# Kernel tuning notes

Measured on AMD Instinct MI355X. Metric: run time of the kernel, lower is better.

The kernel has to match this reference:

```python
import jax, jax.numpy as jnp
import numpy as np

N_NODES = 100000
N_EDGES = 1600000
D = 128          # in_dim == out_dim
H = 8            # num_heads
DH = D // H      # head dim = 16
DFF = 2 * D
EPS_LN = 1e-5


def _ln(x, g, b):
    mu = jnp.mean(x, axis=-1, keepdims=True)
    var = jnp.var(x, axis=-1, keepdims=True)
    return (x - mu) * jax.lax.rsqrt(var + EPS_LN) * g + b


def setup_inputs() -> dict:
    key = jax.random.key(0)
    ks = jax.random.split(key, 12)
    s = 1.0 / np.sqrt(D)
    inp = {
        "h": jax.random.normal(ks[0], (N_NODES, D), jnp.float32),
        "src": jax.random.randint(ks[1], (N_EDGES,), 0, N_NODES, jnp.int32),
        "dst": jax.random.randint(ks[2], (N_EDGES,), 0, N_NODES, jnp.int32),
        "Wq": jax.random.normal(ks[3], (D, D), jnp.float32) * s,
        "Wk": jax.random.normal(ks[4], (D, D), jnp.float32) * s,
        "Wv": jax.random.normal(ks[5], (D, D), jnp.float32) * s,
        "Wo": jax.random.normal(ks[6], (D, D), jnp.float32) * s,
        "bo": jnp.zeros((D,), jnp.float32),
        "ln1_g": jnp.ones((D,), jnp.float32),
        "ln1_b": jnp.zeros((D,), jnp.float32),
        "W1": jax.random.normal(ks[7], (D, DFF), jnp.float32) * s,
        "b1": jnp.zeros((DFF,), jnp.float32),
        "W2": jax.random.normal(ks[8], (DFF, D), jnp.float32) * (1.0 / np.sqrt(DFF)),
        "b2": jnp.zeros((D,), jnp.float32),
        "ln2_g": jnp.ones((D,), jnp.float32),
        "ln2_b": jnp.zeros((D,), jnp.float32),
    }
    return inp


def reference(h, src, dst, Wq, Wk, Wv, Wo, bo, ln1_g, ln1_b, W1, b1, W2, b2, ln2_g, ln2_b):
    n = h.shape[0]
    # Q/K/V projections (no bias), split into heads: [N, H, DH]
    Q = (h @ Wq).reshape(n, H, DH)
    K = (h @ Wk).reshape(n, H, DH)
    V = (h @ Wv).reshape(n, H, DH)

    # edge-wise attention score: K[src] . Q[dst] / sqrt(DH), exp-clamped
    score = jnp.einsum("ehd,ehd->eh", K[src], Q[dst]) / np.sqrt(DH)  # [E, H]
    score = jnp.exp(jnp.clip(score, -5.0, 5.0))

    # weighted message sum + normalizer via segment reduce over dst
    m = V[src] * score[:, :, None]                                   # [E, H, DH]
    wV = jax.ops.segment_sum(m, dst, num_segments=n)                 # [N, H, DH]
    z = jax.ops.segment_sum(score, dst, num_segments=n)              # [N, H]

    h_attn = (wV / (z[:, :, None] + 1e-6)).reshape(n, D)

    # output projection + residual + LN
    x = h + (h_attn @ Wo + bo)
    x = _ln(x, ln1_g, ln1_b)

    # FFN + residual + LN
    y = jax.nn.relu(x @ W1 + b1) @ W2 + b2
    x = _ln(x + y, ln2_g, ln2_b)
    return x
```

## Files before the change

### kernel.cpp

```cpp
#include <hip/hip_runtime.h>
#include <hip/hip_bf16.h>
#include <math.h>


typedef __attribute__((ext_vector_type(8))) short bf16x8;
typedef __attribute__((ext_vector_type(4))) float f32x4;

#define BSHIFT 9
#define BSIZE  512

template<int K, bool AF32, bool RELU, bool LN, bool RESID, bool BIAS, bool YW>
__global__ __launch_bounds__(256)
void gemm_mfma(const void* __restrict__ Ap, int lda,
               const __hip_bfloat16* __restrict__ Bt, int ldbt,
               const float* __restrict__ bias, const float* __restrict__ resid,
               const float* __restrict__ lng, const float* __restrict__ lnb,
               float* __restrict__ Cf, __hip_bfloat16* __restrict__ Cb, int ldc,
               size_t bt_ystride, size_t cb_ystride, int N)
{
    constexpr int CK = 128;
    __shared__ unsigned short As[64 * 136];
    __shared__ unsigned short Bs[128 * 136];

    const int tid  = threadIdx.x;
    const int row0 = blockIdx.x * 64;
    int col0 = 0;
    if (YW) { Bt += blockIdx.y * bt_ystride; Cb += blockIdx.y * cb_ystride; }
    else    col0 = blockIdx.y * 128;

    const int wave = tid >> 6, lane = tid & 63;
    const int quad = lane >> 4, l15 = lane & 15;

    f32x4 acc[8];
    #pragma unroll
    for (int t = 0; t < 8; ++t) acc[t] = (f32x4)0.f;

    for (int kc = 0; kc < K; kc += CK) {
        #pragma unroll
        for (int it = 0; it < 4; ++it) {
            int i = tid + it * 256;
            int r = i >> 4, kb = i & 15;
            int rg = row0 + r; if (rg > N - 1) rg = N - 1;
            if (AF32) {
                const float* Af = (const float*)Ap;
                const float4 f0 = *(const float4*)&Af[(size_t)rg * lda + kc + kb * 8];
                const float4 f1 = *(const float4*)&Af[(size_t)rg * lda + kc + kb * 8 + 4];
                __hip_bfloat162 b01 = __float22bfloat162_rn(make_float2(f0.x, f0.y));
                __hip_bfloat162 b23 = __float22bfloat162_rn(make_float2(f0.z, f0.w));
                __hip_bfloat162 b45 = __float22bfloat162_rn(make_float2(f1.x, f1.y));
                __hip_bfloat162 b67 = __float22bfloat162_rn(make_float2(f1.z, f1.w));
                uint4 u;
                u.x = *(unsigned*)&b01; u.y = *(unsigned*)&b23;
                u.z = *(unsigned*)&b45; u.w = *(unsigned*)&b67;
                *(uint4*)&As[r * 136 + kb * 8] = u;
            } else {
                const __hip_bfloat16* Ab = (const __hip_bfloat16*)Ap;
                *(uint4*)&As[r * 136 + kb * 8] =
                    *(const uint4*)&Ab[(size_t)rg * lda + kc + kb * 8];
            }
        }
        #pragma unroll
        for (int it = 0; it < 8; ++it) {
            int i = tid + it * 256;
            int r = i >> 4, kb = i & 15;
            *(uint4*)&Bs[r * 136 + kb * 8] =
                *(const uint4*)&Bt[(size_t)(col0 + r) * ldbt + kc + kb * 8];
        }
        __syncthreads();
        const unsigned short* ap = &As[(wave * 16 + l15) * 136 + quad * 8];
        const unsigned short* bp = &Bs[l15 * 136 + quad * 8];
        #pragma unroll
        for (int ks = 0; ks < 4; ++ks) {
            bf16x8 a = *(const bf16x8*)(ap + ks * 32);
            #pragma unroll
            for (int t = 0; t < 8; ++t) {
                bf16x8 b = *(const bf16x8*)(bp + t * 16 * 136 + ks * 32);
                acc[t] = __builtin_amdgcn_mfma_f32_16x16x32_bf16(a, b, acc[t], 0, 0, 0);
            }
        }
        __syncthreads();
    }

    const int rbase = row0 + wave * 16 + quad * 4;

    float vals[8][4];
    #pragma unroll
    for (int t = 0; t < 8; ++t) {
        float bv = BIAS ? bias[col0 + t * 16 + l15] : 0.f;
        #pragma unroll
        for (int i = 0; i < 4; ++i) vals[t][i] = acc[t][i] + bv;
    }
    if (RESID) {
        #pragma unroll
        for (int i = 0; i < 4; ++i) {
            int row = rbase + i;
            if (row < N) {
                #pragma unroll
                for (int t = 0; t < 8; ++t)
                    vals[t][i] += resid[(size_t)row * 128 + t * 16 + l15];
            }
        }
    }
    if (RELU) {
        #pragma unroll
        for (int t = 0; t < 8; ++t)
            #pragma unroll
            for (int i = 0; i < 4; ++i) vals[t][i] = fmaxf(vals[t][i], 0.f);
    }
    if (LN) {
        #pragma unroll
        for (int i = 0; i < 4; ++i) {
            float s = 0.f, sq = 0.f;
            #pragma unroll
            for (int t = 0; t < 8; ++t) { float v = vals[t][i]; s += v; sq += v * v; }
            s  += __shfl_xor(s, 1);  s  += __shfl_xor(s, 2);
            s  += __shfl_xor(s, 4);  s  += __shfl_xor(s, 8);
            sq += __shfl_xor(sq, 1); sq += __shfl_xor(sq, 2);
            sq += __shfl_xor(sq, 4); sq += __shfl_xor(sq, 8);
            float m  = s * (1.f / 128.f);
            float rs = rsqrtf(sq * (1.f / 128.f) - m * m + 1e-5f);
            #pragma unroll
            for (int t = 0; t < 8; ++t) {
                float g = lng[t * 16 + l15], b = lnb[t * 16 + l15];
                vals[t][i] = (vals[t][i] - m) * rs * g + b;
            }
        }
    }
    #pragma unroll
    for (int i = 0; i < 4; ++i) {
        int row = rbase + i;
        if (row >= N) continue;
        if (Cf) {
            #pragma unroll
            for (int t = 0; t < 8; ++t)
                Cf[(size_t)row * ldc + col0 + t * 16 + l15] = vals[t][i];
        }
        if (Cb) {
            #pragma unroll
            for (int t = 0; t < 8; ++t)
                Cb[(size_t)row * ldc + col0 + t * 16 + l15] = __float2bfloat16(vals[t][i]);
        }
    }
}

struct WArgs {
    const float* src[6];
    __hip_bfloat16* dst[6];
    int R[6], C[6];
};
__global__ __launch_bounds__(256)
void cast_w(WArgs wa)
{
    int w = blockIdx.y;
    int R = wa.R[w], C = wa.C[w];
    int i = blockIdx.x * 256 + threadIdx.x;
    if (i >= R * C) return;
    int sh = (C == 256) ? 8 : 7;
    int r = i >> sh, c = i & (C - 1);
    wa.dst[w][(size_t)c * R + r] = __float2bfloat16(wa.src[w][i]);
}


__global__ __launch_bounds__(256)
void bucket_hist(const int* __restrict__ dst, int* __restrict__ bCnt,
                 int E, int chunk, int NB)
{
    __shared__ int bh[256];
    const int t = threadIdx.x;
    bh[t] = 0;
    __syncthreads();
    const int s0 = blockIdx.x * chunk;
    const int s1 = min(E, s0 + chunk);
    for (int i = s0 + t; i < s1; i += 256)
        atomicAdd(&bh[dst[i] >> BSHIFT], 1);
    __syncthreads();
    if (t < NB && bh[t]) atomicAdd(&bCnt[t], bh[t]);
}

__global__ __launch_bounds__(256)
void bucket_scan(const int* __restrict__ bCnt, int* __restrict__ bBase,
                 int* __restrict__ gCur, int* __restrict__ rowStart,
                 int N, int E, int NB)
{
    __shared__ int wsum[4];
    const int t = threadIdx.x, lane = t & 63, wv = t >> 6;
    int v = (t < NB) ? bCnt[t] : 0;
    const int s = v;
    for (int off = 1; off < 64; off <<= 1) {
        int u = __shfl_up(v, off);
        if (lane >= off) v += u;
    }
    if (lane == 63) wsum[wv] = v;
    __syncthreads();
    int add = 0;
    for (int w = 0; w < wv; ++w) add += wsum[w];
    const int excl = v + add - s;
    if (t <= NB) bBase[t] = excl;
    if (t < NB)  gCur[t]  = excl;
    if (t == 0)  rowStart[N] = E;
}

__global__ __launch_bounds__(256)
void partition_kernel(const int* __restrict__ src, const int* __restrict__ dst,
                      int* __restrict__ gCur, uint2* __restrict__ P,
                      int E, int chunk, int NB)
{
    __shared__ int ch[256];
    __shared__ int cur[256];
    const int t = threadIdx.x;
    ch[t] = 0;
    __syncthreads();
    const int s0 = blockIdx.x * chunk;
    const int s1 = min(E, s0 + chunk);
    for (int i = s0 + t; i < s1; i += 256)
        atomicAdd(&ch[dst[i] >> BSHIFT], 1);
    __syncthreads();
    if (t < NB) {
        int c = ch[t];
        cur[t] = c ? atomicAdd(&gCur[t], c) : 0;
    }
    __syncthreads();
    for (int i = s0 + t; i < s1; i += 256) {
        int d = dst[i];
        int pos = atomicAdd(&cur[d >> BSHIFT], 1);
        P[pos] = make_uint2((unsigned)src[i], (unsigned)d);
    }
}

__global__ __launch_bounds__(256)
void bucket_scatter(const uint2* __restrict__ P, const int* __restrict__ bBase,
                    int* __restrict__ rowStart, int* __restrict__ esrc, int N)
{
    __shared__ int hist[BSIZE];
    __shared__ int cur[BSIZE];
    __shared__ int wsum[4];

    const int b  = blockIdx.x;
    const int t  = threadIdx.x;
    const int d0 = b << BSHIFT;
    const int bb  = bBase[b];
    const int cnt = bBase[b + 1] - bb;

    hist[t] = 0; hist[t + 256] = 0;
    __syncthreads();
    for (int i = t; i < cnt; i += 256)
        atomicAdd(&hist[(int)P[bb + i].y - d0], 1);
    __syncthreads();

    {
        const int a0 = hist[2 * t], a1 = hist[2 * t + 1];
        int v = a0 + a1;
        const int s = v;
        const int lane = t & 63, wv = t >> 6;
        for (int off = 1; off < 64; off <<= 1) {
            int u = __shfl_up(v, off);
            if (lane >= off) v += u;
        }
        if (lane == 63) wsum[wv] = v;
        __syncthreads();
        int add = 0;
        for (int w = 0; w < wv; ++w) add += wsum[w];
        const int exclT = v + add - s;
        cur[2 * t]     = exclT;
        cur[2 * t + 1] = exclT + a0;
    }
    __syncthreads();
    for (int i = t; i < BSIZE; i += 256) {
        int d = d0 + i;
        if (d < N) rowStart[d] = bb + cur[i];
    }
    __syncthreads();
    for (int i = t; i < cnt; i += 256) {
        uint2 p = P[bb + i];
        int pos = atomicAdd(&cur[(int)p.y - d0], 1);
        esrc[bb + pos] = (int)p.x;
    }
}

__global__ __launch_bounds__(256)
void aggregate_kernel(__hip_bfloat16* __restrict__ Q,
                      const __hip_bfloat16* __restrict__ Km,
                      const __hip_bfloat16* __restrict__ V,
                      const int* __restrict__ esrc,
                      const int* __restrict__ rowStart, int N)
{
    const int lane = threadIdx.x & 63;
    const int wid  = threadIdx.x >> 6;
    const int d    = blockIdx.x * 4 + wid;
    if (d >= N) return;

    const int l5   = lane & 31;
    const int half = lane >> 5;

    const uint2* K2 = (const uint2*)Km;
    const uint2* V2 = (const uint2*)V;
    uint2*       Q2 = (uint2*)Q;

    const uint2 qraw = Q2[(unsigned)d * 32u + (unsigned)l5];
    const float q0 = __uint_as_float(qraw.x << 16);
    const float q1 = __uint_as_float(qraw.x & 0xffff0000u);
    const float q2 = __uint_as_float(qraw.y << 16);
    const float q3 = __uint_as_float(qraw.y & 0xffff0000u);

    const int beg = rowStart[d];
    const int end = rowStart[d + 1];

    float a0 = 0.f, a1 = 0.f, a2 = 0.f, a3 = 0.f, zacc = 0.f;
    const float S = 0.36067376022224085f;
    const float C = 7.2134752044448170f;

    for (int base = beg; base < end; base += 64) {
        int n = end - base; if (n > 64) n = 64;
        int mysrc = (lane < n) ? esrc[base + lane] : 0;
        const int nf = n >> 1;
        int bidx = half;
        for (int j = 0; j < nf; ++j, bidx += 2) {
            const int s = __shfl(mysrc, bidx);
            const unsigned off = (unsigned)s * 32u + (unsigned)l5;
            const uint2 kraw = K2[off];
            const uint2 vraw = V2[off];
            float p = __uint_as_float(kraw.x << 16)         * q0
                    + __uint_as_float(kraw.x & 0xffff0000u) * q1
                    + __uint_as_float(kraw.y << 16)         * q2
                    + __uint_as_float(kraw.y & 0xffff0000u) * q3;
            p += __shfl_xor(p, 1);
            p += __shfl_xor(p, 2);
            const float tt = fminf(C, fmaxf(-C, p * S));
            const float se = exp2f(tt);
            a0 += __uint_as_float(vraw.x << 16)         * se;
            a1 += __uint_as_float(vraw.x & 0xffff0000u) * se;
            a2 += __uint_as_float(vraw.y << 16)         * se;
            a3 += __uint_as_float(vraw.y & 0xffff0000u) * se;
            zacc += se;
        }
        if (n & 1) {
            const int s = __shfl(mysrc, n - 1);
            const unsigned off = (unsigned)s * 32u + (unsigned)l5;
            const uint2 kraw = K2[off];
            const uint2 vraw = V2[off];
            float p = __uint_as_float(kraw.x << 16)         * q0
                    + __uint_as_float(kraw.x & 0xffff0000u) * q1
                    + __uint_as_float(kraw.y << 16)         * q2
                    + __uint_as_float(kraw.y & 0xffff0000u) * q3;
            p += __shfl_xor(p, 1);
            p += __shfl_xor(p, 2);
            const float tt = fminf(C, fmaxf(-C, p * S));
            float se = exp2f(tt);
            se = half ? 0.f : se;
            a0 += __uint_as_float(vraw.x << 16)         * se;
            a1 += __uint_as_float(vraw.x & 0xffff0000u) * se;
            a2 += __uint_as_float(vraw.y << 16)         * se;
            a3 += __uint_as_float(vraw.y & 0xffff0000u) * se;
            zacc += se;
        }
    }

    a0 += __shfl_xor(a0, 32); a1 += __shfl_xor(a1, 32);
    a2 += __shfl_xor(a2, 32); a3 += __shfl_xor(a3, 32);
    zacc += __shfl_xor(zacc, 32);

    if (half == 0) {
        const float inv = 1.0f / (zacc + 1e-6f);
        __hip_bfloat162 p0 = __float22bfloat162_rn(make_float2(a0 * inv, a1 * inv));
        __hip_bfloat162 p1 = __float22bfloat162_rn(make_float2(a2 * inv, a3 * inv));
        uint2 o;
        o.x = *(unsigned*)&p0;
        o.y = *(unsigned*)&p1;
        Q2[(unsigned)d * 32u + (unsigned)l5] = o;
    }
}

extern "C" void kernel_launch(void* const* d_in, const int* in_sizes, int n_in,
                              void* d_out, int out_size, void* d_ws, size_t ws_size,
                              hipStream_t stream)
{
    const float* h    = (const float*)d_in[0];
    const int*   src  = (const int*)  d_in[1];
    const int*   dst  = (const int*)  d_in[2];
    const float* Wq   = (const float*)d_in[3];
    const float* Wk   = (const float*)d_in[4];
    const float* Wv   = (const float*)d_in[5];
    const float* Wo   = (const float*)d_in[6];
    const float* bo   = (const float*)d_in[7];
    const float* ln1g = (const float*)d_in[8];
    const float* ln1b = (const float*)d_in[9];
    const float* W1   = (const float*)d_in[10];
    const float* b1   = (const float*)d_in[11];
    const float* W2   = (const float*)d_in[12];
    const float* b2   = (const float*)d_in[13];
    const float* ln2g = (const float*)d_in[14];
    const float* ln2b = (const float*)d_in[15];

    const int N = in_sizes[0] / 128;
    const int E = in_sizes[1];
    const int NB = (N + BSIZE - 1) >> BSHIFT;

    __hip_bfloat16* Qh = (__hip_bfloat16*)d_ws;
    __hip_bfloat16* Kh = Qh + (size_t)N * 128;
    __hip_bfloat16* Vh = Kh + (size_t)N * 128;
    __hip_bfloat16* Xh = Vh + (size_t)N * 128;
    float*          Xf = (float*)(Xh + (size_t)N * 128);
    __hip_bfloat16* Wt = (__hip_bfloat16*)(Xf + (size_t)N * 128);
    __hip_bfloat16* Wqt = Wt;
    __hip_bfloat16* Wkt = Wqt + 16384;
    __hip_bfloat16* Wvt = Wkt + 16384;
    __hip_bfloat16* Wot = Wvt + 16384;
    __hip_bfloat16* W1t = Wot + 16384;
    __hip_bfloat16* W2t = W1t + 32768;
    int* ib       = (int*)(W2t + 32768);
    int* bCnt     = ib;
    int* bBase    = ib + 256;
    int* gCur     = ib + 514;
    int* rowStart = ib + 770;
    int* esrc     = ib + 770 + N + 2;
    uint2* P      = (uint2*)Xf;
    __hip_bfloat16* Th = Qh;

    const dim3 blk(256);
    const int  nb    = (N + 63) / 64;
    const int  chunk = (E + 255) / 256;

    WArgs wa;
    wa.src[0] = Wq; wa.src[1] = Wk; wa.src[2] = Wv; wa.src[3] = Wo; wa.src[4] = W1; wa.src[5] = W2;
    wa.dst[0] = Wqt; wa.dst[1] = Wkt; wa.dst[2] = Wvt; wa.dst[3] = Wot; wa.dst[4] = W1t; wa.dst[5] = W2t;
    wa.R[0] = wa.R[1] = wa.R[2] = wa.R[3] = 128; wa.R[4] = 128; wa.R[5] = 256;
    wa.C[0] = wa.C[1] = wa.C[2] = wa.C[3] = 128; wa.C[4] = 256; wa.C[5] = 128;
    cast_w<<<dim3(128, 6), blk, 0, stream>>>(wa);

    gemm_mfma<128,true,false,false,false,false,true><<<dim3(nb, 3), blk, 0, stream>>>(
        h, 128, Wqt, 128, nullptr, nullptr, nullptr, nullptr,
        nullptr, Qh, 128, (size_t)16384, (size_t)N * 128, N);

    hipMemsetAsync(bCnt, 0, 256 * sizeof(int), stream);
    bucket_hist<<<dim3(256), blk, 0, stream>>>(dst, bCnt, E, chunk, NB);
    bucket_scan<<<dim3(1), blk, 0, stream>>>(bCnt, bBase, gCur, rowStart, N, E, NB);
    partition_kernel<<<dim3(256), blk, 0, stream>>>(src, dst, gCur, P, E, chunk, NB);
    bucket_scatter<<<dim3(NB), blk, 0, stream>>>(P, bBase, rowStart, esrc, N);

    aggregate_kernel<<<dim3((N + 3) / 4), blk, 0, stream>>>(Qh, Kh, Vh, esrc, rowStart, N);

    gemm_mfma<128,false,false,true,true,true,false><<<dim3(nb, 1), blk, 0, stream>>>(
        Qh, 128, Wot, 128, bo, h, ln1g, ln1b, Xf, Xh, 128, 0, 0, N);

    gemm_mfma<128,false,true,false,false,true,false><<<dim3(nb, 2), blk, 0, stream>>>(
        Xh, 128, W1t, 128, b1, nullptr, nullptr, nullptr, nullptr, Th, 256, 0, 0, N);

    gemm_mfma<256,false,false,true,true,true,false><<<dim3(nb, 1), blk, 0, stream>>>(
        Th, 256, W2t, 256, b2, Xf, ln2g, ln2b, (float*)d_out, nullptr, 128, 0, 0, N);
}
```

Measured before the change: 423.6 us.

## Interleave K and V per head, drop fp32 LN1 intermediate

The QKV projection now writes K and V into one interleaved buffer, placing each lane's 4 K values next to its 4 V values. The edge aggregation can then fetch both with a single 16-byte gather per edge instead of two 8-byte gathers, and its inner loop is unrolled by two. The fp32 copy of the first LayerNorm output is removed, and the final GEMM reads its residual from the bf16 copy. This cuts memory traffic and workspace size, at the cost of a small loss of residual precision and more complex output indexing in the projection epilogue.

```diff
diff --git a/kernel.cpp b/kernel.cpp
--- a/kernel.cpp
+++ b/kernel.cpp
@@ -9,14 +9,15 @@
 #define BSHIFT 9
 #define BSIZE  512
 
-template<int K, bool AF32, bool RELU, bool LN, bool RESID, bool BIAS, bool YW>
+template<int K, bool AF32, bool RELU, bool LN, bool RESID, bool RESB, bool BIAS, bool YW>
 __global__ __launch_bounds__(256)
 void gemm_mfma(const void* __restrict__ Ap, int lda,
                const __hip_bfloat16* __restrict__ Bt, int ldbt,
-               const float* __restrict__ bias, const float* __restrict__ resid,
+               const float* __restrict__ bias, const void* __restrict__ resid,
                const float* __restrict__ lng, const float* __restrict__ lnb,
-               float* __restrict__ Cf, __hip_bfloat16* __restrict__ Cb, int ldc,
-               size_t bt_ystride, size_t cb_ystride, int N)
+               float* __restrict__ Cf, __hip_bfloat16* __restrict__ Cb,
+               __hip_bfloat16* __restrict__ Cb2, int ldc,
+               size_t bt_ystride, int N)
 {
     constexpr int CK = 128;
     __shared__ unsigned short As[64 * 136];
@@ -25,7 +26,7 @@
     const int tid  = threadIdx.x;
     const int row0 = blockIdx.x * 64;
     int col0 = 0;
-    if (YW) { Bt += blockIdx.y * bt_ystride; Cb += blockIdx.y * cb_ystride; }
+    if (YW) Bt += blockIdx.y * bt_ystride;
     else    col0 = blockIdx.y * 128;
 
     const int wave = tid >> 6, lane = tid & 63;
@@ -90,14 +91,46 @@
         #pragma unroll
         for (int i = 0; i < 4; ++i) vals[t][i] = acc[t][i] + bv;
     }
+
+    if (YW) {
+        const int y = blockIdx.y;
+        #pragma unroll
+        for (int i = 0; i < 4; ++i) {
+            int row = rbase + i;
+            if (row >= N) continue;
+            if (y == 0) {
+                #pragma unroll
+                for (int t = 0; t < 8; ++t)
+                    Cb[(size_t)row * 128 + t * 16 + l15] = __float2bfloat16(vals[t][i]);
+            } else {
+                const int vo = (y == 2) ? 4 : 0;
+                #pragma unroll
+                for (int t = 0; t < 8; ++t) {
+                    int c = t * 16 + l15;
+                    Cb2[(size_t)row * 256 + ((c >> 2) << 3) + (c & 3) + vo] =
+                        __float2bfloat16(vals[t][i]);
+                }
+            }
+        }
+        return;
+    }
+
     if (RESID) {
         #pragma unroll
         for (int i = 0; i < 4; ++i) {
             int row = rbase + i;
             if (row < N) {
-                #pragma unroll
-                for (int t = 0; t < 8; ++t)
-                    vals[t][i] += resid[(size_t)row * 128 + t * 16 + l15];
+                if (RESB) {
+                    const __hip_bfloat16* rb = (const __hip_bfloat16*)resid;
+                    #pragma unroll
+                    for (int t = 0; t < 8; ++t)
+                        vals[t][i] += __bfloat162float(rb[(size_t)row * 128 + t * 16 + l15]);
+                } else {
+                    const float* rf = (const float*)resid;
+                    #pragma unroll
+                    for (int t = 0; t < 8; ++t)
+                        vals[t][i] += rf[(size_t)row * 128 + t * 16 + l15];
+                }
             }
         }
     }
@@ -159,7 +192,6 @@
     int r = i >> sh, c = i & (C - 1);
     wa.dst[w][(size_t)c * R + r] = __float2bfloat16(wa.src[w][i]);
 }
-
 
 __global__ __launch_bounds__(256)
 void bucket_hist(const int* __restrict__ dst, int* __restrict__ bCnt,
@@ -279,8 +311,7 @@
 
 __global__ __launch_bounds__(256)
 void aggregate_kernel(__hip_bfloat16* __restrict__ Q,
-                      const __hip_bfloat16* __restrict__ Km,
-                      const __hip_bfloat16* __restrict__ V,
+                      const __hip_bfloat16* __restrict__ KV,
                       const int* __restrict__ esrc,
                       const int* __restrict__ rowStart, int N)
 {
@@ -292,9 +323,8 @@
     const int l5   = lane & 31;
     const int half = lane >> 5;
 
-    const uint2* K2 = (const uint2*)Km;
-    const uint2* V2 = (const uint2*)V;
-    uint2*       Q2 = (uint2*)Q;
+    const uint4* KV4 = (const uint4*)KV;
+    uint2*       Q2  = (uint2*)Q;
 
     const uint2 qraw = Q2[(unsigned)d * 32u + (unsigned)l5];
     const float q0 = __uint_as_float(qraw.x << 16);
@@ -314,43 +344,40 @@
         int mysrc = (lane < n) ? esrc[base + lane] : 0;
         const int nf = n >> 1;
         int bidx = half;
+        #pragma unroll 2
         for (int j = 0; j < nf; ++j, bidx += 2) {
             const int s = __shfl(mysrc, bidx);
-            const unsigned off = (unsigned)s * 32u + (unsigned)l5;
-            const uint2 kraw = K2[off];
-            const uint2 vraw = V2[off];
-            float p = __uint_as_float(kraw.x << 16)         * q0
-                    + __uint_as_float(kraw.x & 0xffff0000u) * q1
-                    + __uint_as_float(kraw.y << 16)         * q2
-                    + __uint_as_float(kraw.y & 0xffff0000u) * q3;
+            const uint4 kv = KV4[(unsigned)s * 32u + (unsigned)l5];
+            float p = __uint_as_float(kv.x << 16)         * q0
+                    + __uint_as_float(kv.x & 0xffff0000u) * q1
+                    + __uint_as_float(kv.y << 16)         * q2
+                    + __uint_as_float(kv.y & 0xffff0000u) * q3;
             p += __shfl_xor(p, 1);
             p += __shfl_xor(p, 2);
             const float tt = fminf(C, fmaxf(-C, p * S));
             const float se = exp2f(tt);
-            a0 += __uint_as_float(vraw.x << 16)         * se;
-            a1 += __uint_as_float(vraw.x & 0xffff0000u) * se;
-            a2 += __uint_as_float(vraw.y << 16)         * se;
-            a3 += __uint_as_float(vraw.y & 0xffff0000u) * se;
+            a0 += __uint_as_float(kv.z << 16)         * se;
+            a1 += __uint_as_float(kv.z & 0xffff0000u) * se;
+            a2 += __uint_as_float(kv.w << 16)         * se;
+            a3 += __uint_as_float(kv.w & 0xffff0000u) * se;
             zacc += se;
         }
         if (n & 1) {
             const int s = __shfl(mysrc, n - 1);
-            const unsigned off = (unsigned)s * 32u + (unsigned)l5;
-            const uint2 kraw = K2[off];
-            const uint2 vraw = V2[off];
-            float p = __uint_as_float(kraw.x << 16)         * q0
-                    + __uint_as_float(kraw.x & 0xffff0000u) * q1
-                    + __uint_as_float(kraw.y << 16)         * q2
-                    + __uint_as_float(kraw.y & 0xffff0000u) * q3;
+            const uint4 kv = KV4[(unsigned)s * 32u + (unsigned)l5];
+            float p = __uint_as_float(kv.x << 16)         * q0
+                    + __uint_as_float(kv.x & 0xffff0000u) * q1
+                    + __uint_as_float(kv.y << 16)         * q2
+                    + __uint_as_float(kv.y & 0xffff0000u) * q3;
             p += __shfl_xor(p, 1);
             p += __shfl_xor(p, 2);
             const float tt = fminf(C, fmaxf(-C, p * S));
             float se = exp2f(tt);
             se = half ? 0.f : se;
-            a0 += __uint_as_float(vraw.x << 16)         * se;
-            a1 += __uint_as_float(vraw.x & 0xffff0000u) * se;
-            a2 += __uint_as_float(vraw.y << 16)         * se;
-            a3 += __uint_as_float(vraw.y & 0xffff0000u) * se;
+            a0 += __uint_as_float(kv.z << 16)         * se;
+            a1 += __uint_as_float(kv.z & 0xffff0000u) * se;
+            a2 += __uint_as_float(kv.w << 16)         * se;
+            a3 += __uint_as_float(kv.w & 0xffff0000u) * se;
             zacc += se;
         }
     }
@@ -395,12 +422,10 @@
     const int E = in_sizes[1];
     const int NB = (N + BSIZE - 1) >> BSHIFT;
 
-    __hip_bfloat16* Qh = (__hip_bfloat16*)d_ws;
-    __hip_bfloat16* Kh = Qh + (size_t)N * 128;
-    __hip_bfloat16* Vh = Kh + (size_t)N * 128;
-    __hip_bfloat16* Xh = Vh + (size_t)N * 128;
-    float*          Xf = (float*)(Xh + (size_t)N * 128);
-    __hip_bfloat16* Wt = (__hip_bfloat16*)(Xf + (size_t)N * 128);
+    __hip_bfloat16* Qh  = (__hip_bfloat16*)d_ws;
+    __hip_bfloat16* KVh = Qh + (size_t)N * 128;
+    __hip_bfloat16* Xh  = KVh + (size_t)N * 256;
+    __hip_bfloat16* Wt  = Xh + (size_t)N * 128;
     __hip_bfloat16* Wqt = Wt;
     __hip_bfloat16* Wkt = Wqt + 16384;
     __hip_bfloat16* Wvt = Wkt + 16384;
@@ -413,8 +438,8 @@
     int* gCur     = ib + 514;
     int* rowStart = ib + 770;
     int* esrc     = ib + 770 + N + 2;
-    uint2* P      = (uint2*)Xf;
-    __hip_bfloat16* Th = Qh;
+    uint2* P      = (uint2*)(esrc + E);
+    __hip_bfloat16* Th = KVh;
 
     const dim3 blk(256);
     const int  nb    = (N + 63) / 64;
@@ -427,9 +452,9 @@
     wa.C[0] = wa.C[1] = wa.C[2] = wa.C[3] = 128; wa.C[4] = 256; wa.C[5] = 128;
     cast_w<<<dim3(128, 6), blk, 0, stream>>>(wa);
 
-    gemm_mfma<128,true,false,false,false,false,true><<<dim3(nb, 3), blk, 0, stream>>>(
+    gemm_mfma<128,true,false,false,false,false,false,true><<<dim3(nb, 3), blk, 0, stream>>>(
         h, 128, Wqt, 128, nullptr, nullptr, nullptr, nullptr,
-        nullptr, Qh, 128, (size_t)16384, (size_t)N * 128, N);
+        nullptr, Qh, KVh, 128, (size_t)16384, N);
 
     hipMemsetAsync(bCnt, 0, 256 * sizeof(int), stream);
     bucket_hist<<<dim3(256), blk, 0, stream>>>(dst, bCnt, E, chunk, NB);
@@ -437,14 +462,14 @@
     partition_kernel<<<dim3(256), blk, 0, stream>>>(src, dst, gCur, P, E, chunk, NB);
     bucket_scatter<<<dim3(NB), blk, 0, stream>>>(P, bBase, rowStart, esrc, N);
 
-    aggregate_kernel<<<dim3((N + 3) / 4), blk, 0, stream>>>(Qh, Kh, Vh, esrc, rowStart, N);
-
-    gemm_mfma<128,false,false,true,true,true,false><<<dim3(nb, 1), blk, 0, stream>>>(
-        Qh, 128, Wot, 128, bo, h, ln1g, ln1b, Xf, Xh, 128, 0, 0, N);
-
-    gemm_mfma<128,false,true,false,false,true,false><<<dim3(nb, 2), blk, 0, stream>>>(
-        Xh, 128, W1t, 128, b1, nullptr, nullptr, nullptr, nullptr, Th, 256, 0, 0, N);
-
-    gemm_mfma<256,false,false,true,true,true,false><<<dim3(nb, 1), blk, 0, stream>>>(
-        Th, 256, W2t, 256, b2, Xf, ln2g, ln2b, (float*)d_out, nullptr, 128, 0, 0, N);
-}
+    aggregate_kernel<<<dim3((N + 3) / 4), blk, 0, stream>>>(Qh, KVh, esrc, rowStart, N);
+
+    gemm_mfma<128,false,false,true,true,false,true,false><<<dim3(nb, 1), blk, 0, stream>>>(
+        Qh, 128, Wot, 128, bo, h, ln1g, ln1b, nullptr, Xh, nullptr, 128, 0, N);
+
+    gemm_mfma<128,false,true,false,false,false,true,false><<<dim3(nb, 2), blk, 0, stream>>>(
+        Xh, 128, W1t, 128, b1, nullptr, nullptr, nullptr, nullptr, Th, nullptr, 256, 0, N);
+
+    gemm_mfma<256,false,false,true,true,true,true,false><<<dim3(nb, 1), blk, 0, stream>>>(
+        Th, 256, W2t, 256, b2, Xh, ln2g, ln2b, (float*)d_out, nullptr, nullptr, 128, 0, N);
+}
```

Result: no change. 429.6 us (+1.4%).
